# Optimization experiments

Hardware: AMD Instinct MI355X
Metric: run time of the kernel (lower is better)

## Reference

```python
import jax, jax.numpy as jnp
import numpy as np

B, F, R, P, C = 2048, 64, 32, 16, 128  # batch, nfeature(dsym), nrole, npattern, dcontext
TAU = 2.0  # posn_attender sharpness


def setup_inputs() -> dict:
    key = jax.random.key(0)
    ks = jax.random.split(key, 16)
    w = lambda k, shape, s=0.05: jax.random.normal(k, shape, jnp.float32) * s
    z = lambda shape: jnp.zeros(shape, jnp.float32)
    return {
        "form": jax.random.normal(ks[0], (B, F, R), jnp.float32),
        "context": jax.random.normal(ks[1], (B, C), jnp.float32),
        "mod_W": w(ks[2], (C, P * 6)), "mod_b": z((P * 6,)),
        "wch_W": w(ks[3], (C, P * F)), "wch_b": z((P * F,)),
        "wdl_W": w(ks[4], (C, P)), "wdl_b": z((P,)),
        "wep_W": w(ks[5], (C, P * 4)), "wep_b": z((P * 4,)),
        "vch_W": w(ks[6], (C, P * F)), "vch_b": z((P * F,)),
        "vep_W": w(ks[7], (C, P * F * 4)), "vep_b": z((P * F * 4,)),
        "wnc_W": w(ks[8], (C, F)), "wnc_b": z((F,)),
        "wnd_W": w(ks[9], (C, 1)), "wnd_b": z((1,)),
        "wne_W": w(ks[10], (C, 1)), "wne_b": z((1,)),
        "m_W": w(ks[11], (3, C, P * F)), "m_Wb": z((3, P * F)),
        "mb_W": w(ks[12], (3, C, P)), "mb_b": z((3, P)),
    }


def _forward(form, context, mod_W, mod_b, wch_W, wch_b, wdl_W, wdl_b,
             wep_W, wep_b, vch_W, vch_b, vep_W, vep_b,
             wnc_W, wnc_b, wnd_W, wnd_b, wne_W, wne_b,
             m_W, m_Wb, mb_W, mb_b):
    nb = form.shape[0]
    lin = lambda W, b: context @ W + b

    # context-conditioned rule weights
    mod = jax.nn.softmax(lin(mod_W, mod_b).reshape(nb, P, 6), axis=-1)
    w_chng = mod[..., 0:1] * lin(wch_W, wch_b).reshape(nb, P, F)
    w_deln = mod[..., 1:2] * lin(wdl_W, wdl_b).reshape(nb, P, 1)
    w_epen = mod[..., 2:] * lin(wep_W, wep_b).reshape(nb, P, 4)
    v_chng = lin(vch_W, vch_b).reshape(nb, P, F)
    v_epen = lin(vep_W, vep_b).reshape(nb, P, F, 4)
    w_nochng = jnp.exp(lin(wnc_W, wnc_b))   # (B, F)
    w_nodeln = jnp.exp(lin(wnd_W, wnd_b))   # (B, 1)
    w_noepen = jnp.exp(lin(wne_W, wne_b))   # (B, 1)

    # Matcher3: trigram (prev, cur, next) feature matching; log-prob summed then exp'd
    prev = jnp.pad(form[:, :, :-1], ((0, 0), (0, 0), (1, 0)))
    nxt = jnp.pad(form[:, :, 1:], ((0, 0), (0, 0), (0, 1)))
    forms3 = jnp.stack([prev, form, nxt], 0)                                   # (3,B,F,R)
    Wk = (jnp.einsum('bc,kcn->kbn', context, m_W) + m_Wb[:, None, :]).reshape(3, nb, P, F)
    bk = jnp.einsum('bc,kcp->kbp', context, mb_W) + mb_b[:, None, :]
    score = jnp.einsum('kbpf,kbfr->kbpr', Wk, forms3) + bk[..., None]
    match = jnp.exp(jnp.sum(jax.nn.log_sigmoid(score), axis=0))                # (B,P,R)

    positions = jnp.arange(R, dtype=form.dtype)

    def posn_attn(posn):  # (B,1) soft position -> (B,R) radial-basis attention
        return jax.nn.softmax(-TAU * (posn - positions[None, :]) ** 2, axis=-1)

    def bind(out, x, attn):  # soft write symbol x at attended role
        a = attn[:, None, :]
        return out * (1.0 - a) + x[:, :, None] * a

    def epen(out, posn, match_i, we_p, ve_p):
        we = match_i * we_p                                                    # (B,P)
        p = jax.nn.sigmoid(jnp.sum(we, 1, keepdims=True) - w_noepen)           # (B,1)
        v = jnp.sum(jax.nn.relu(we)[..., None] * ve_p, 1)                      # (B,F)
        out_ = bind(out, v, posn_attn(posn))
        out = p[..., None] * out_ + (1.0 - p[..., None]) * out
        return out, posn + p

    def step(carry, x):
        out, posn = carry
        sym_i, match_i = x  # (B,F), (B,P)
        # epenthesis before
        out, posn = epen(out, posn, match_i, w_epen[..., 0], v_epen[..., 0])
        # feature change + deletion
        wc = match_i[..., None] * w_chng                                       # (B,P,F)
        p_chng = jax.nn.sigmoid(jnp.sum(wc, 1) - w_nochng)                     # (B,F)
        vc = jnp.sum(jax.nn.relu(wc) * v_chng, 1)                              # (B,F)
        sym = sym_i + p_chng * (vc - sym_i)
        out_ = bind(out, sym, posn_attn(posn))
        wd = match_i[..., None] * w_deln                                       # (B,P,1)
        p_deln = jax.nn.sigmoid(jnp.sum(wd, 1) - w_nodeln)                     # (B,1)
        out = (1.0 - p_deln[..., None]) * out_ + p_deln[..., None] * out
        posn = posn + (1.0 - p_deln)
        # epenthesis after
        out, posn = epen(out, posn, match_i, w_epen[..., 2], v_epen[..., 2])
        return (out, posn), None

    carry0 = (jnp.zeros((nb, F, R), form.dtype), jnp.zeros((nb, 1), form.dtype))
    xs = (jnp.moveaxis(form, 2, 0), jnp.moveaxis(match, 2, 0))
    (out, _), _ = jax.lax.scan(step, carry0, xs)
    return out


def reference(form, context, mod_W, mod_b, wch_W, wch_b, wdl_W, wdl_b,
              wep_W, wep_b, vch_W, vch_b, vep_W, vep_b,
              wnc_W, wnc_b, wnd_W, wnd_b, wne_W, wne_b,
              m_W, m_Wb, mb_W, mb_b):
    return _forward(form, context, mod_W, mod_b, wch_W, wch_b, wdl_W, wdl_b,
                    wep_W, wep_b, vch_W, vch_b, vep_W, vep_b,
                    wnc_W, wnc_b, wnd_W, wnd_b, wne_W, wne_b,
                    m_W, m_Wb, mb_W, mb_b)
```

## Files before the change

kernel.cpp:

```cpp
#include <hip/hip_runtime.h>

#define B_ 2048
#define YS3 7440
#define NT  465

typedef unsigned short u16;
typedef unsigned int   u32;
typedef __attribute__((ext_vector_type(2))) float v2f;
typedef __attribute__((ext_vector_type(8))) short bf16x8;
typedef __attribute__((ext_vector_type(4))) float f32x4;

__device__ __forceinline__ float bfu(u16 u) {
    u32 i = ((u32)u) << 16; float f; __builtin_memcpy(&f, &i, 4); return f;
}
__device__ __forceinline__ u16 f2bf(float v) {
    u32 iv; __builtin_memcpy(&iv, &v, 4);
    u32 r = (iv + 0x7fffu + ((iv >> 16) & 1u)) >> 16;
    return (u16)r;
}
__device__ __forceinline__ float sigm(float x) { return 1.f / (1.f + __expf(-x)); }
__device__ __forceinline__ float lsg(float x) {
    return fminf(x, 0.f) - log1pf(__expf(-fabsf(x)));
}

template<bool F32> __device__ __forceinline__ float LD(const void* p, int e) {
    if (F32) return ((const float*)p)[e];
    return bfu(((const u16*)p)[e]);
}
template<bool F32> __device__ __forceinline__ float2 LD2(const void* p, int e) {
    if (F32) { const float* q = (const float*)p; return make_float2(q[e], q[e + 1]); }
    u32 w = ((const u32*)p)[e >> 1];
    u32 lo = w << 16, hi = w & 0xffff0000u; float a, b;
    __builtin_memcpy(&a, &lo, 4); __builtin_memcpy(&b, &hi, 4);
    return make_float2(a, b);
}
template<bool F32> __device__ __forceinline__ float4 LD4(const void* p, int e) {
    if (F32) return ((const float4*)p)[e >> 2];
    uint2 w = ((const uint2*)p)[e >> 2];
    u32 a0 = w.x << 16, a1 = w.x & 0xffff0000u, a2 = w.y << 16, a3 = w.y & 0xffff0000u;
    float f0, f1, f2, f3;
    __builtin_memcpy(&f0, &a0, 4); __builtin_memcpy(&f1, &a1, 4);
    __builtin_memcpy(&f2, &a2, 4); __builtin_memcpy(&f3, &a3, 4);
    return make_float4(f0, f1, f2, f3);
}
template<bool F32> __device__ __forceinline__ void ST(void* p, int e, float v) {
    if (F32) ((float*)p)[e] = v; else ((u16*)p)[e] = f2bf(v);
}

struct Args {
    const void *form, *ctx;
    const void *mod_W, *mod_b, *wch_W, *wch_b, *wdl_W, *wdl_b, *wep_W, *wep_b;
    const void *vch_W, *vch_b, *vep_W, *vep_b;
    const void *wnc_W, *wnc_b, *wnd_W, *wnd_b, *wne_W, *wne_b;
    const void *m_W, *m_Wb, *mb_W, *mb_b;
    void* outp;
};

__device__ __forceinline__ int probe_is_f32(const void* ctx, int t, int* flag_s) {
    if (t == 0) {
        int sane = 0;
        const u16* q = (const u16*)ctx;
        for (int i = 0; i < 64; ++i) {
            u16 u = q[2 * i];
            int ex = (u >> 7) & 0xFF;
            sane += (u == 0 || (ex >= 112 && ex <= 143)) ? 1 : 0;
        }
        *flag_s = (sane < 32) ? 1 : 0;
    }
    __syncthreads();
    return *flag_s;
}

__device__ __forceinline__ void split_bf16(float x, u16& hi, u16& lo) {
    hi = f2bf(x);
    lo = f2bf(x - bfu(hi));
}


template<bool F32>
__device__ void packw_body(int g, const Args& A, u16* Bpack, float* bcat) {
    int l  = g & 63;
    int kb = (g >> 6) & 3;
    int T  = g >> 8;
    int n  = T * 16 + (l & 15);
    int k0 = kb * 32 + (l >> 4) * 8;

    const void* p = A.wch_W; int off = 0, st = 0, zero = 0; float bb = 0.f;
    if (n < 1024)      { off = n; st = 1024; bb = LD<F32>(A.wch_b, n); }
    else if (n < 2048) { int j = n - 1024; p = A.vch_W; off = j; st = 1024; bb = LD<F32>(A.vch_b, j); }
    else if (n < 4096) { int i = n - 2048; int col = 4 * (i >> 1) + 2 * (i & 1);
                         p = A.vep_W; off = col; st = 4096; bb = LD<F32>(A.vep_b, col); }
    else if (n < 7168) { int i = n - 4096; int kk = i >> 10, j = i & 1023;
                         p = A.m_W; off = kk * 131072 + j; st = 1024; bb = LD<F32>(A.m_Wb, kk * 1024 + j); }
    else if (n < 7264) { int m = n - 7168; p = A.mod_W; off = m; st = 96; bb = LD<F32>(A.mod_b, m); }
    else if (n < 7312) { int i = n - 7264; int k = i >> 4, pp = i & 15;
                         p = A.mb_W; off = k * 2048 + pp; st = 16; bb = LD<F32>(A.mb_b, k * 16 + pp); }
    else if (n < 7344) { int i = n - 7312; int col = 4 * (i >> 1) + 2 * (i & 1);
                         p = A.wep_W; off = col; st = 64; bb = LD<F32>(A.wep_b, col); }
    else if (n < 7360) { int j = n - 7344; p = A.wdl_W; off = j; st = 16; bb = LD<F32>(A.wdl_b, j); }
    else if (n < 7424) { int j = n - 7360; p = A.wnc_W; off = j; st = 64; bb = LD<F32>(A.wnc_b, j); }
    else if (n == 7424){ p = A.wnd_W; off = 0; st = 1; bb = LD<F32>(A.wnd_b, 0); }
    else if (n == 7425){ p = A.wne_W; off = 0; st = 1; bb = LD<F32>(A.wne_b, 0); }
    else zero = 1;

    u16 hi[8], lo[8];
    #pragma unroll
    for (int j = 0; j < 8; ++j) {
        float w = LD<F32>(p, off + (k0 + j) * st);
        if (zero) w = 0.f;
        split_bf16(w, hi[j], lo[j]);
    }
    *(uint4*)(Bpack + ((size_t)T * 512 + kb * 64 + l) * 8)       = *(const uint4*)hi;
    *(uint4*)(Bpack + ((size_t)T * 512 + 256 + kb * 64 + l) * 8) = *(const uint4*)lo;
    if (kb == 0 && l < 16) bcat[n] = zero ? 0.f : bb;
}

__global__ __launch_bounds__(256) void packw_kernel(Args A, u16* Bpack, float* bcat) {
    __shared__ int dt_s;
    const int t = threadIdx.x;
    int isf32 = probe_is_f32(A.ctx, t, &dt_s);
    int g = blockIdx.x * 256 + t;
    if (isf32) packw_body<true>(g, A, Bpack, bcat);
    else       packw_body<false>(g, A, Bpack, bcat);
}

template<bool F32>
__device__ void gemm_mfma_body(float* As, int t, int blk, const void* __restrict__ ctx,
                               const u16* __restrict__ Bpack,
                               const float* __restrict__ bcat, float* __restrict__ Y) {
    const int l  = t & 63;
    const int w  = t >> 6;
    const int Mt = blk & 127;
    const int nb = blk >> 7;

    {
        int row = t >> 4, c0 = (t & 15) * 8;
        float4 x = LD4<F32>(ctx, (Mt * 16 + row) * 128 + c0);
        float4 y = LD4<F32>(ctx, (Mt * 16 + row) * 128 + c0 + 4);
        *(float4*)&As[row * 132 + c0]     = x;
        *(float4*)&As[row * 132 + c0 + 4] = y;
    }
    __syncthreads();

    bf16x8 ahi[4], alo[4];
    const int m = l & 15;
    #pragma unroll
    for (int kb = 0; kb < 4; ++kb) {
        int k0 = kb * 32 + (l >> 4) * 8;
        const float* ap = &As[m * 132 + k0];
        #pragma unroll
        for (int j = 0; j < 8; ++j) {
            u16 hi, lo; split_bf16(ap[j], hi, lo);
            ahi[kb][j] = (short)hi;
            alo[kb][j] = (short)lo;
        }
    }

    const int Tbase = nb * 16 + w * 4;
    const int row0  = Mt * 16 + (l >> 4) * 4;
    const int ncol  = l & 15;

    #pragma unroll
    for (int T = 0; T < 4; ++T) {
        int Tt = Tbase + T;
        if (Tt >= NT) break;
        const u16* Bb = Bpack + (size_t)Tt * 4096;
        bf16x8 bhi[4], blo[4];
        #pragma unroll
        for (int kb = 0; kb < 4; ++kb) {
            bhi[kb] = *(const bf16x8*)(Bb + ((kb) * 64 + l) * 8);
            blo[kb] = *(const bf16x8*)(Bb + ((4 + kb) * 64 + l) * 8);
        }
        f32x4 d = {0.f, 0.f, 0.f, 0.f};
        #pragma unroll
        for (int kb = 0; kb < 4; ++kb) {
            d = __builtin_amdgcn_mfma_f32_16x16x32_bf16(ahi[kb], bhi[kb], d, 0, 0, 0);
            d = __builtin_amdgcn_mfma_f32_16x16x32_bf16(ahi[kb], blo[kb], d, 0, 0, 0);
            d = __builtin_amdgcn_mfma_f32_16x16x32_bf16(alo[kb], bhi[kb], d, 0, 0, 0);
        }
        int n = Tt * 16 + ncol;
        float bv = bcat[n];
        #pragma unroll
        for (int i = 0; i < 4; ++i) {
            Y[(size_t)(row0 + i) * YS3 + n] = d[i] + bv;
        }
    }
}

__global__ __launch_bounds__(256) void gemm_mfma_kernel(Args A, const u16* Bpack,
                                                        const float* bcat, float* Y) {
    __shared__ float As[16 * 132];
    __shared__ int dt_s;
    const int t = threadIdx.x, blk = blockIdx.x;
    int isf32 = probe_is_f32(A.ctx, t, &dt_s);
    if (isf32) gemm_mfma_body<true>(As, t, blk, A.ctx, Bpack, bcat, Y);
    else       gemm_mfma_body<false>(As, t, blk, A.ctx, Bpack, bcat, Y);
}

struct __align__(16) ScanSmem {
    float U[6144];
    float V[3072];
    float match_s[512];
    float wnc_s[64];
    float wep0_s[16], wep2_s[16], wdl_s[16];
    float coef_s[96];
    float sc_s[2];
};

template<bool F32>
__device__ void scan_body(ScanSmem& S, int t, int b, const Args& A, const float* __restrict__ Y) {
    float* Wk_s   = S.U;
    float* bk_s   = S.U + 3072;
    float* modl   = S.U + 3120;
    float* form_s = S.U + 3312;
    float* xtab   = S.U;
    float* wch_s  = S.V;
    float* vch_s  = S.V + 1024;
    float* rlI    = S.V + 2048;
    float* gtab   = S.V;

    const float* Yr = Y + (size_t)b * YS3;
    const float4* Y4 = (const float4*)Yr;

    const int f_own = t & 63;
    const int fq    = t >> 6;

    const float2* vep2p = (const float2*)(Yr + 2048);
    v2f vepf[16];
    #pragma unroll
    for (int p = 0; p < 16; ++p) {
        float2 v = vep2p[p * 64 + f_own];
        vepf[p].x = v.x; vepf[p].y = v.y;
    }

    {
        int e0 = b * 2048 + t * 8;
        float4 x = LD4<F32>(A.form, e0);
        float4 y = LD4<F32>(A.form, e0 + 4);
        int f = t >> 2, r0 = (t & 3) * 8;
        float* dst = form_s + f * 33 + r0;
        dst[0] = x.x; dst[1] = x.y; dst[2] = x.z; dst[3] = x.w;
        dst[4] = y.x; dst[5] = y.y; dst[6] = y.z; dst[7] = y.w;
    }
    for (int i = t; i < 768; i += 256) ((float4*)Wk_s)[i] = Y4[1024 + i];
    if (t < 12) ((float4*)bk_s)[t] = Y4[1816 + t];
    if (t < 24) ((float4*)modl)[t] = Y4[1792 + t];
    ((float4*)wch_s)[t] = Y4[t];
    ((float4*)vch_s)[t] = Y4[256 + t];
    if (t < 16) {
        S.wep0_s[t] = Yr[7312 + 2 * t];
        S.wep2_s[t] = Yr[7312 + 2 * t + 1];
        S.wdl_s[t]  = Yr[7344 + t];
    } else if (t >= 32 && t < 96) {
        S.wnc_s[t - 32] = __expf(Yr[7360 + (t - 32)]);
    } else if (t >= 96 && t < 98) {
        S.sc_s[t - 96] = __expf(Yr[7424 + (t - 96)]);
    }
    __syncthreads();

    if (t < 16) {
        float v[6]; float mx = -1e30f;
        #pragma unroll
        for (int j = 0; j < 6; ++j) { v[j] = modl[t * 6 + j]; mx = fmaxf(mx, v[j]); }
        float s = 0.f;
        #pragma unroll
        for (int j = 0; j < 6; ++j) { v[j] = __expf(v[j] - mx); s += v[j]; }
        float inv = 1.f / s;
        #pragma unroll
        for (int j = 0; j < 6; ++j) modl[t * 6 + j] = v[j] * inv;
    }
    __syncthreads();

    if (t < 16) {
        S.wep0_s[t] *= modl[t * 6 + 2];
        S.wep2_s[t] *= modl[t * 6 + 4];
        S.wdl_s[t]  *= modl[t * 6 + 1];
    }
    for (int i = t; i < 1024; i += 256) wch_s[i] *= modl[(i >> 6) * 6];

    const int my_r = t & 31;
    #pragma unroll 1
    for (int it = 0; it < 2; ++it) {
        int idx = t + 256 * it;
        int p = idx >> 5, r = idx & 31;
        float s0 = bk_s[p], s1 = bk_s[16 + p], s2 = bk_s[32 + p];
        const float4* w0 = (const float4*)(Wk_s + p * 64);
        const float4* w1 = (const float4*)(Wk_s + (16 + p) * 64);
        const float4* w2 = (const float4*)(Wk_s + (32 + p) * 64);
        for (int f4 = 0; f4 < 16; ++f4) {
            float a0[4], a1[4], a2[4];
            *(float4*)a0 = w0[f4]; *(float4*)a1 = w1[f4]; *(float4*)a2 = w2[f4];
            #pragma unroll
            for (int j = 0; j < 4; ++j) {
                int f = f4 * 4 + j;
                float f0 = form_s[f * 33 + r];
                float fm = __shfl_up(f0, 1, 32);   if (r == 0)  fm = 0.f;
                float fp = __shfl_down(f0, 1, 32); if (r == 31) fp = 0.f;
                s0 += a0[j] * fm; s1 += a1[j] * f0; s2 += a2[j] * fp;
            }
        }
        S.match_s[p * 32 + r] = __expf(lsg(s0) + lsg(s1) + lsg(s2));
    }
    __syncthreads();

    if (t < 96) {
        int sub = t >> 5, r = t & 31;
        const float* w = (sub == 0) ? S.wep0_s : (sub == 1) ? S.wdl_s : S.wep2_s;
        float s = 0.f;
        for (int p = 0; p < 16; ++p) s += S.match_s[p * 32 + r] * w[p];
        float cf;
        if (sub == 1) cf = 1.f - sigm(s - S.sc_s[0]);
        else          cf = sigm(s - S.sc_s[1]);
        S.coef_s[sub * 32 + r] = cf;
    }
    for (int i = t; i < 512; i += 256) {
        int p = i >> 5, r = i & 31;
        float m = S.match_s[p * 32 + r];
        rlI[2 * i]     = fmaxf(m * S.wep0_s[p], 0.f);
        rlI[2 * i + 1] = fmaxf(m * S.wep2_s[p], 0.f);
    }
    float wchf[16], vchf[16];
    #pragma unroll
    for (int p = 0; p < 16; ++p) {
        wchf[p] = wch_s[p * 64 + f_own];
        vchf[p] = vch_s[p * 64 + f_own];
    }
    const float wncf = S.wnc_s[f_own];
    float si_r[8];
    #pragma unroll
    for (int j = 0; j < 8; ++j) si_r[j] = form_s[f_own * 33 + fq * 8 + j];
    __syncthreads();

    #pragma unroll 1
    for (int j = 0; j < 8; ++j) {
        int rs = fq * 8 + j;
        v2f v02; v02.x = 0.f; v02.y = 0.f;
        float sum = 0.f, vs1 = 0.f;
        const v2f* rlp = (const v2f*)(rlI + 2 * rs);
        #pragma unroll
        for (int p = 0; p < 16; ++p) {
            v2f rl = rlp[p * 32];
            v02 += rl * vepf[p];
            float m = S.match_s[p * 32 + rs];
            float wc = m * wchf[p];
            sum += wc;
            vs1 += fmaxf(wc, 0.f) * vchf[p];
        }
        float pch = sigm(sum - wncf);
        float si  = si_r[j];
        xtab[0 * 2048 + rs * 64 + f_own] = v02.x;
        xtab[1 * 2048 + rs * 64 + f_own] = si + pch * (vs1 - si);
        xtab[2 * 2048 + rs * 64 + f_own] = v02.y;
    }
    __syncthreads();

    float* ck_s  = S.match_s;
    float* pos_s = S.match_s + 128;
    if (t < 96) ck_s[t] = S.coef_s[(t % 3) * 32 + (t / 3)];
    __syncthreads();
    if (t < 64) {
        float a = ck_s[t];
        float a0 = a;
        #pragma unroll
        for (int d = 1; d < 64; d <<= 1) { float v = __shfl_up(a, d, 64); if (t >= d) a += v; }
        pos_s[t] = a - a0;
        float carry = __shfl(a, 63, 64);
        float b2 = (t < 32) ? ck_s[64 + t] : 0.f;
        float c2 = b2;
        #pragma unroll
        for (int d = 1; d < 32; d <<= 1) { float v = __shfl_up(c2, d, 32); if ((t & 31) >= d) c2 += v; }
        if (t < 32) pos_s[64 + t] = carry + c2 - b2;
    }
    __syncthreads();

    #pragma unroll 1
    for (int i = 0; i < 12; ++i) {
        int idx = t + 256 * i;
        int k = idx >> 5, r = idx & 31;
        float posn = pos_s[k];
        float pc = fminf(posn, 31.f);
        float ci = floorf(pc + 0.5f);
        float dmin = posn - ci;
        float dd = posn - (float)r;
        float eo = __expf(-2.f * (dd * dd - dmin * dmin));
        float Z = eo;
        Z += __shfl_xor(Z, 1, 32);
        Z += __shfl_xor(Z, 2, 32);
        Z += __shfl_xor(Z, 4, 32);
        Z += __shfl_xor(Z, 8, 32);
        Z += __shfl_xor(Z, 16, 32);
        gtab[idx] = ck_s[k] * eo / Z;
    }
    __syncthreads();

    const int fgrp = t >> 5;
    v2f o01, o23, o45, o67;
    o01 = 0.f; o23 = 0.f; o45 = 0.f; o67 = 0.f;
    #pragma unroll 1
    for (int rs = 0; rs < 32; ++rs) {
        #pragma unroll
        for (int sub = 0; sub < 3; ++sub) {
            float g = gtab[(rs * 3 + sub) * 32 + my_r];
            v2f gv; gv.x = g; gv.y = g;
            const float4* xb = (const float4*)(xtab + sub * 2048 + rs * 64 + fgrp * 8);
            float4 xa = xb[0], xc = xb[1];
            v2f x01, x23, x45, x67;
            x01.x = xa.x; x01.y = xa.y; x23.x = xa.z; x23.y = xa.w;
            x45.x = xc.x; x45.y = xc.y; x67.x = xc.z; x67.y = xc.w;
            o01 += gv * (x01 - o01);
            o23 += gv * (x23 - o23);
            o45 += gv * (x45 - o45);
            o67 += gv * (x67 - o67);
        }
    }

    float oreg[8] = {o01.x, o01.y, o23.x, o23.y, o45.x, o45.y, o67.x, o67.y};
    #pragma unroll
    for (int i = 0; i < 8; ++i) {
        ST<F32>(A.outp, b * 2048 + (fgrp * 8 + i) * 32 + my_r, oreg[i]);
    }
}

__global__ __launch_bounds__(256) void scan_kernel(Args A, const float* Y) {
    __shared__ ScanSmem S;
    __shared__ int dt_s;
    const int t = threadIdx.x, b = blockIdx.x;
    int isf32 = probe_is_f32(A.ctx, t, &dt_s);
    if (isf32) scan_body<true>(S, t, b, A, Y);
    else       scan_body<false>(S, t, b, A, Y);
}

struct Smem {
    float U[6144];
    float form_s[64 * 33];
    float match_s[512];
    float wch_s[1024];
    float vch_s[1024];
    float vep0_s[1024];
    float vep2_s[1024];
    float wep0_s[16], wep2_s[16], wdl_s[16];
    float wnc_s[64];
    float sc_s[2];
    float ssum_s[96];
};

template<bool F32>
__device__ void mono_body(Smem& S, int t, int b, const Args& A) {
    float* c_s  = S.U;
    float* modl = S.U + 128;
    float* Wk_s = S.U + 224;
    float* bk_s = S.U + 3344;
    float* xtab = S.U;

    if (t < 128) c_s[t] = LD<F32>(A.ctx, b * 128 + t);
    {
        int e0 = b * 2048 + t * 8;
        float4 x = LD4<F32>(A.form, e0);
        float4 y = LD4<F32>(A.form, e0 + 4);
        int f = t >> 2, r0 = (t & 3) * 8;
        float* dst = S.form_s + f * 33 + r0;
        dst[0] = x.x; dst[1] = x.y; dst[2] = x.z; dst[3] = x.w;
        dst[4] = y.x; dst[5] = y.y; dst[6] = y.z; dst[7] = y.w;
    }
    __syncthreads();
    if (t < 96) {
        float a = LD<F32>(A.mod_b, t);
        for (int cc = 0; cc < 128; ++cc) a += c_s[cc] * LD<F32>(A.mod_W, cc * 96 + t);
        modl[t] = a;
    }
    __syncthreads();
    if (t < 16) {
        float v[6]; float mx = -1e30f;
        #pragma unroll
        for (int j = 0; j < 6; ++j) { v[j] = modl[t * 6 + j]; mx = fmaxf(mx, v[j]); }
        float s = 0.f;
        #pragma unroll
        for (int j = 0; j < 6; ++j) { v[j] = __expf(v[j] - mx); s += v[j]; }
        float inv = 1.f / s;
        #pragma unroll
        for (int j = 0; j < 6; ++j) modl[t * 6 + j] = v[j] * inv;
    }
    __syncthreads();
    for (int j = t; j < 512; j += 256) {
        int n0 = j * 2;
        float2 bb = LD2<F32>(A.wch_b, n0);
        float a0 = bb.x, a1 = bb.y;
        for (int cc = 0; cc < 128; ++cc) {
            float2 w = LD2<F32>(A.wch_W, cc * 1024 + n0); float cv = c_s[cc];
            a0 += cv * w.x; a1 += cv * w.y;
        }
        int p = n0 >> 6; float sc = modl[p * 6 + 0];
        S.wch_s[n0] = sc * a0; S.wch_s[n0 + 1] = sc * a1;
    }
    for (int j = t; j < 512; j += 256) {
        int n0 = j * 2;
        float2 bb = LD2<F32>(A.vch_b, n0);
        float a0 = bb.x, a1 = bb.y;
        for (int cc = 0; cc < 128; ++cc) {
            float2 w = LD2<F32>(A.vch_W, cc * 1024 + n0); float cv = c_s[cc];
            a0 += cv * w.x; a1 += cv * w.y;
        }
        S.vch_s[n0] = a0; S.vch_s[n0 + 1] = a1;
    }
    for (int u = t; u < 1024; u += 256) {
        int n0 = u * 4;
        float4 bb = LD4<F32>(A.vep_b, n0);
        float a0 = bb.x, a2 = bb.z;
        for (int cc = 0; cc < 128; ++cc) {
            float4 w = LD4<F32>(A.vep_W, cc * 4096 + n0); float cv = c_s[cc];
            a0 += cv * w.x; a2 += cv * w.z;
        }
        S.vep0_s[u] = a0; S.vep2_s[u] = a2;
    }
    for (int j = t; j < 1536; j += 256) {
        int k  = j >> 9;
        int jj = j & 511;
        int n0 = jj * 2;
        float2 bb = LD2<F32>(A.m_Wb, k * 1024 + n0);
        float a0 = bb.x, a1 = bb.y;
        for (int cc = 0; cc < 128; ++cc) {
            float2 w = LD2<F32>(A.m_W, (k * 128 + cc) * 1024 + n0); float cv = c_s[cc];
            a0 += cv * w.x; a1 += cv * w.y;
        }
        int p = n0 >> 6, f = n0 & 63;
        Wk_s[(k * 16 + p) * 65 + f]     = a0;
        Wk_s[(k * 16 + p) * 65 + f + 1] = a1;
    }
    if (t < 16) {
        int n0 = t * 4;
        float4 bb = LD4<F32>(A.wep_b, n0);
        float a0 = bb.x, a2 = bb.z;
        for (int cc = 0; cc < 128; ++cc) {
            float4 w = LD4<F32>(A.wep_W, cc * 64 + n0); float cv = c_s[cc];
            a0 += cv * w.x; a2 += cv * w.z;
        }
        S.wep0_s[t] = modl[t * 6 + 2] * a0;
        S.wep2_s[t] = modl[t * 6 + 4] * a2;
    } else if (t < 32) {
        int p = t - 16;
        float a = LD<F32>(A.wdl_b, p);
        for (int cc = 0; cc < 128; ++cc) a += c_s[cc] * LD<F32>(A.wdl_W, cc * 16 + p);
        S.wdl_s[p] = modl[p * 6 + 1] * a;
    } else if (t < 96) {
        int f = t - 32;
        float a = LD<F32>(A.wnc_b, f);
        for (int cc = 0; cc < 128; ++cc) a += c_s[cc] * LD<F32>(A.wnc_W, cc * 64 + f);
        S.wnc_s[f] = __expf(a);
    } else if (t < 98) {
        const void* W  = (t == 96) ? A.wnd_W : A.wne_W;
        const void* bb = (t == 96) ? A.wnd_b : A.wne_b;
        float a = LD<F32>(bb, 0);
        for (int cc = 0; cc < 128; ++cc) a += c_s[cc] * LD<F32>(W, cc);
        S.sc_s[t - 96] = __expf(a);
    } else if (t < 146) {
        int i = t - 98;
        int k = i >> 4, p = i & 15;
        float a = LD<F32>(A.mb_b, k * 16 + p);
        for (int cc = 0; cc < 128; ++cc) a += c_s[cc] * LD<F32>(A.mb_W, (k * 128 + cc) * 16 + p);
        bk_s[i] = a;
    }
    __syncthreads();
    for (int idx = t; idx < 512; idx += 256) {
        int p = idx >> 5, r = idx & 31;
        float s0 = bk_s[p], s1 = bk_s[16 + p], s2 = bk_s[32 + p];
        const float* w0 = Wk_s + p * 65;
        const float* w1 = Wk_s + (16 + p) * 65;
        const float* w2 = Wk_s + (32 + p) * 65;
        for (int f = 0; f < 64; ++f) {
            const float* fr = S.form_s + f * 33 + r;
            float fm1 = (r > 0)  ? fr[-1] : 0.f;
            float f0  = fr[0];
            float fp1 = (r < 31) ? fr[1]  : 0.f;
            s0 += w0[f] * fm1; s1 += w1[f] * f0; s2 += w2[f] * fp1;
        }
        S.match_s[p * 32 + r] = __expf(lsg(s0) + lsg(s1) + lsg(s2));
    }
    __syncthreads();
    if (t < 96) {
        int which = t >> 5, r = t & 31;
        const float* w = (which == 0) ? S.wep0_s : (which == 1) ? S.wep2_s : S.wdl_s;
        float s = 0.f;
        for (int p = 0; p < 16; ++p) s += S.match_s[p * 32 + r] * w[p];
        S.ssum_s[which * 32 + r] = s;
    }
    #pragma unroll 1
    for (int q = 0; q < 24; ++q) {
        int idx = t + 256 * q;
        int sub = idx >> 11;
        int rs  = (idx >> 6) & 31;
        int f   = idx & 63;
        float x;
        if (sub == 1) {
            float sum = 0.f, vs = 0.f;
            for (int p = 0; p < 16; ++p) {
                float wc = S.match_s[p * 32 + rs] * S.wch_s[p * 64 + f];
                sum += wc;
                vs  += fmaxf(wc, 0.f) * S.vch_s[p * 64 + f];
            }
            float pch = sigm(sum - S.wnc_s[f]);
            float si  = S.form_s[f * 33 + rs];
            x = si + pch * (vs - si);
        } else {
            const float* wep = (sub == 0) ? S.wep0_s : S.wep2_s;
            const float* vep = (sub == 0) ? S.vep0_s : S.vep2_s;
            float vs = 0.f;
            for (int p = 0; p < 16; ++p) {
                float w = S.match_s[p * 32 + rs] * wep[p];
                vs += fmaxf(w, 0.f) * vep[p * 64 + f];
            }
            x = vs;
        }
        xtab[idx] = x;
    }
    __syncthreads();
    const int my_r = t & 31;
    const int fgrp = t >> 5;
    float oreg[8];
    #pragma unroll
    for (int i = 0; i < 8; ++i) oreg[i] = 0.f;
    float posn = 0.f;
    const float wnd1v = S.sc_s[0];
    const float wne1v = S.sc_s[1];
    for (int rs = 0; rs < 32; ++rs) {
        #pragma unroll
        for (int sub = 0; sub < 3; ++sub) {
            float coef;
            if (sub == 1) coef = 1.f - sigm(S.ssum_s[64 + rs] - wnd1v);
            else          coef = sigm(S.ssum_s[(sub & 2) * 16 + rs] - wne1v);
            float pc = fminf(posn, 31.f);
            int ci = (int)(pc + 0.5f);
            int lo = ci - 4; if (lo < 0)  lo = 0;
            int hi = ci + 4; if (hi > 31) hi = 31;
            float dmin = posn - (float)ci;
            float mx = -2.f * dmin * dmin;
            float Z = 0.f, eo = 0.f;
            for (int r = lo; r <= hi; ++r) {
                float d = posn - (float)r;
                float e = __expf(-2.f * d * d - mx);
                Z += e;
                if (r == my_r) eo = e;
            }
            float g = coef * eo / Z;
            const float* xb = xtab + (sub * 2048 + rs * 64 + fgrp * 8);
            #pragma unroll
            for (int i = 0; i < 8; ++i) oreg[i] += g * (xb[i] - oreg[i]);
            posn += coef;
        }
    }
    #pragma unroll
    for (int i = 0; i < 8; ++i) {
        ST<F32>(A.outp, b * 2048 + (fgrp * 8 + i) * 32 + my_r, oreg[i]);
    }
}

__global__ __launch_bounds__(256) void phon_mono(Args A) {
    __shared__ Smem S;
    __shared__ int dt_s;
    const int t = threadIdx.x, b = blockIdx.x;
    int isf32 = probe_is_f32(A.ctx, t, &dt_s);
    if (isf32) mono_body<true>(S, t, b, A);
    else       mono_body<false>(S, t, b, A);
}

extern "C" void kernel_launch(void* const* d_in, const int* in_sizes, int n_in,
                              void* d_out, int out_size, void* d_ws, size_t ws_size,
                              hipStream_t stream) {
    Args A;
    A.form  = d_in[0];  A.ctx   = d_in[1];
    A.mod_W = d_in[2];  A.mod_b = d_in[3];
    A.wch_W = d_in[4];  A.wch_b = d_in[5];
    A.wdl_W = d_in[6];  A.wdl_b = d_in[7];
    A.wep_W = d_in[8];  A.wep_b = d_in[9];
    A.vch_W = d_in[10]; A.vch_b = d_in[11];
    A.vep_W = d_in[12]; A.vep_b = d_in[13];
    A.wnc_W = d_in[14]; A.wnc_b = d_in[15];
    A.wnd_W = d_in[16]; A.wnd_b = d_in[17];
    A.wne_W = d_in[18]; A.wne_b = d_in[19];
    A.m_W   = d_in[20]; A.m_Wb  = d_in[21];
    A.mb_W  = d_in[22]; A.mb_b  = d_in[23];
    A.outp  = d_out;

    const size_t yElems  = (size_t)B_ * YS3;
    const size_t bpElems = (size_t)NT * 4096;
    const size_t need = yElems * 4 + bpElems * 2 + (size_t)YS3 * 4;
    if (ws_size >= need) {
        float* Y     = (float*)d_ws;
        u16*   Bpack = (u16*)(Y + yElems);
        float* bcat  = (float*)(Bpack + bpElems);
        packw_kernel<<<NT, 256, 0, stream>>>(A, Bpack, bcat);
        gemm_mfma_kernel<<<30 * 128, 256, 0, stream>>>(A, Bpack, bcat, Y);
        scan_kernel<<<B_, 256, 0, stream>>>(A, Y);
    } else {
        phon_mono<<<B_, 256, 0, stream>>>(A);
    }
}
```

Before: 243.8 us.

## Compute trigram matcher with split-bf16 MFMA and vectorize xtab accumulation

Replaces the scalar FMA/shuffle trigram matching loop with 16x16x32 bf16 MFMAs, using hi/lo bf16 splitting (three products) to keep near-fp32 accuracy. Matcher weights are now read straight from global memory instead of being staged in shared memory, and form_s is padded with zero columns so the shifted prev/next operands need no shuffles. The per-rs loop that builds xtab is restructured to accumulate all 8 rows at once with float4 LDS reads, and the vep register loads are moved later to ease register pressure. The cost is extra conversion arithmetic and the small error of the three-term bf16 split.

```diff
diff --git a/kernel.cpp b/kernel.cpp
--- a/kernel.cpp
+++ b/kernel.cpp
@@ -209,10 +209,9 @@
 
 template<bool F32>
 __device__ void scan_body(ScanSmem& S, int t, int b, const Args& A, const float* __restrict__ Y) {
-    float* Wk_s   = S.U;
-    float* bk_s   = S.U + 3072;
-    float* modl   = S.U + 3120;
-    float* form_s = S.U + 3312;
+    float* bk_s   = S.U;
+    float* modl   = S.U + 48;
+    float* form_s = S.U + 144;
     float* xtab   = S.U;
     float* wch_s  = S.V;
     float* vch_s  = S.V + 1024;
@@ -224,37 +223,33 @@
 
     const int f_own = t & 63;
     const int fq    = t >> 6;
-
-    const float2* vep2p = (const float2*)(Yr + 2048);
-    v2f vepf[16];
-    #pragma unroll
-    for (int p = 0; p < 16; ++p) {
-        float2 v = vep2p[p * 64 + f_own];
-        vepf[p].x = v.x; vepf[p].y = v.y;
-    }
-
+    const int l     = t & 63;
+    const int wv    = t >> 6;
+    const int my_r  = t & 31;
+
+    if (t < 64) { form_s[t * 34] = 0.f; form_s[t * 34 + 33] = 0.f; }
     {
         int e0 = b * 2048 + t * 8;
         float4 x = LD4<F32>(A.form, e0);
         float4 y = LD4<F32>(A.form, e0 + 4);
         int f = t >> 2, r0 = (t & 3) * 8;
-        float* dst = form_s + f * 33 + r0;
+        float* dst = form_s + f * 34 + 1 + r0;
         dst[0] = x.x; dst[1] = x.y; dst[2] = x.z; dst[3] = x.w;
         dst[4] = y.x; dst[5] = y.y; dst[6] = y.z; dst[7] = y.w;
     }
-    for (int i = t; i < 768; i += 256) ((float4*)Wk_s)[i] = Y4[1024 + i];
     if (t < 12) ((float4*)bk_s)[t] = Y4[1816 + t];
-    if (t < 24) ((float4*)modl)[t] = Y4[1792 + t];
+    else if (t >= 32 && t < 56) ((float4*)modl)[t - 32] = Y4[1792 + (t - 32)];
     ((float4*)wch_s)[t] = Y4[t];
     ((float4*)vch_s)[t] = Y4[256 + t];
-    if (t < 16) {
-        S.wep0_s[t] = Yr[7312 + 2 * t];
-        S.wep2_s[t] = Yr[7312 + 2 * t + 1];
-        S.wdl_s[t]  = Yr[7344 + t];
-    } else if (t >= 32 && t < 96) {
-        S.wnc_s[t - 32] = __expf(Yr[7360 + (t - 32)]);
-    } else if (t >= 96 && t < 98) {
-        S.sc_s[t - 96] = __expf(Yr[7424 + (t - 96)]);
+    if (t >= 64 && t < 80) {
+        int p = t - 64;
+        S.wep0_s[p] = Yr[7312 + 2 * p];
+        S.wep2_s[p] = Yr[7312 + 2 * p + 1];
+        S.wdl_s[p]  = Yr[7344 + p];
+    } else if (t >= 96 && t < 160) {
+        S.wnc_s[t - 96] = __expf(Yr[7360 + (t - 96)]);
+    } else if (t >= 160 && t < 162) {
+        S.sc_s[t - 160] = __expf(Yr[7424 + (t - 160)]);
     }
     __syncthreads();
 
@@ -278,28 +273,46 @@
     }
     for (int i = t; i < 1024; i += 256) wch_s[i] *= modl[(i >> 6) * 6];
 
-    const int my_r = t & 31;
-    #pragma unroll 1
-    for (int it = 0; it < 2; ++it) {
-        int idx = t + 256 * it;
-        int p = idx >> 5, r = idx & 31;
-        float s0 = bk_s[p], s1 = bk_s[16 + p], s2 = bk_s[32 + p];
-        const float4* w0 = (const float4*)(Wk_s + p * 64);
-        const float4* w1 = (const float4*)(Wk_s + (16 + p) * 64);
-        const float4* w2 = (const float4*)(Wk_s + (32 + p) * 64);
-        for (int f4 = 0; f4 < 16; ++f4) {
-            float a0[4], a1[4], a2[4];
-            *(float4*)a0 = w0[f4]; *(float4*)a1 = w1[f4]; *(float4*)a2 = w2[f4];
+    if (wv < 2) {
+        const int q  = l >> 4;
+        const int rb = wv * 16 + (l & 15);
+        f32x4 msum = {0.f, 0.f, 0.f, 0.f};
+        #pragma unroll
+        for (int kmat = 0; kmat < 3; ++kmat) {
+            f32x4 d = {0.f, 0.f, 0.f, 0.f};
             #pragma unroll
-            for (int j = 0; j < 4; ++j) {
-                int f = f4 * 4 + j;
-                float f0 = form_s[f * 33 + r];
-                float fm = __shfl_up(f0, 1, 32);   if (r == 0)  fm = 0.f;
-                float fp = __shfl_down(f0, 1, 32); if (r == 31) fp = 0.f;
-                s0 += a0[j] * fm; s1 += a1[j] * f0; s2 += a2[j] * fp;
+            for (int kb = 0; kb < 2; ++kb) {
+                const float* ap = Yr + 4096 + kmat * 1024 + (l & 15) * 64 + kb * 32 + q * 8;
+                float4 a0 = *(const float4*)ap;
+                float4 a1 = *(const float4*)(ap + 4);
+                float av[8] = {a0.x, a0.y, a0.z, a0.w, a1.x, a1.y, a1.z, a1.w};
+                bf16x8 Ahi, Alo, Bhi, Blo;
+                #pragma unroll
+                for (int j = 0; j < 8; ++j) {
+                    u16 hi, lo; split_bf16(av[j], hi, lo);
+                    Ahi[j] = (short)hi; Alo[j] = (short)lo;
+                }
+                int coladdr = rb + kmat;
+                #pragma unroll
+                for (int j = 0; j < 8; ++j) {
+                    int f = kb * 32 + q * 8 + j;
+                    float v = form_s[f * 34 + coladdr];
+                    u16 hi, lo; split_bf16(v, hi, lo);
+                    Bhi[j] = (short)hi; Blo[j] = (short)lo;
+                }
+                d = __builtin_amdgcn_mfma_f32_16x16x32_bf16(Ahi, Bhi, d, 0, 0, 0);
+                d = __builtin_amdgcn_mfma_f32_16x16x32_bf16(Ahi, Blo, d, 0, 0, 0);
+                d = __builtin_amdgcn_mfma_f32_16x16x32_bf16(Alo, Bhi, d, 0, 0, 0);
             }
-        }
-        S.match_s[p * 32 + r] = __expf(lsg(s0) + lsg(s1) + lsg(s2));
+            #pragma unroll
+            for (int i = 0; i < 4; ++i) {
+                msum[i] += lsg(d[i] + bk_s[kmat * 16 + q * 4 + i]);
+            }
+        }
+        #pragma unroll
+        for (int i = 0; i < 4; ++i) {
+            S.match_s[(q * 4 + i) * 32 + rb] = __expf(msum[i]);
+        }
     }
     __syncthreads();
 
@@ -319,6 +332,13 @@
         rlI[2 * i]     = fmaxf(m * S.wep0_s[p], 0.f);
         rlI[2 * i + 1] = fmaxf(m * S.wep2_s[p], 0.f);
     }
+    const float2* vep2p = (const float2*)(Yr + 2048);
+    v2f vepf[16];
+    #pragma unroll
+    for (int p = 0; p < 16; ++p) {
+        float2 v = vep2p[p * 64 + f_own];
+        vepf[p].x = v.x; vepf[p].y = v.y;
+    }
     float wchf[16], vchf[16];
     #pragma unroll
     for (int p = 0; p < 16; ++p) {
@@ -328,29 +348,41 @@
     const float wncf = S.wnc_s[f_own];
     float si_r[8];
     #pragma unroll
-    for (int j = 0; j < 8; ++j) si_r[j] = form_s[f_own * 33 + fq * 8 + j];
-    __syncthreads();
-
-    #pragma unroll 1
-    for (int j = 0; j < 8; ++j) {
-        int rs = fq * 8 + j;
-        v2f v02; v02.x = 0.f; v02.y = 0.f;
-        float sum = 0.f, vs1 = 0.f;
-        const v2f* rlp = (const v2f*)(rlI + 2 * rs);
+    for (int j = 0; j < 8; ++j) si_r[j] = form_s[f_own * 34 + 1 + fq * 8 + j];
+    __syncthreads();
+
+    {
+        v2f v02[8]; float sum[8], vs1[8];
+        #pragma unroll
+        for (int j = 0; j < 8; ++j) { v02[j].x = 0.f; v02[j].y = 0.f; sum[j] = 0.f; vs1[j] = 0.f; }
+        const float4* m4  = (const float4*)S.match_s;
+        const float4* rl4 = (const float4*)rlI;
         #pragma unroll
         for (int p = 0; p < 16; ++p) {
-            v2f rl = rlp[p * 32];
-            v02 += rl * vepf[p];
-            float m = S.match_s[p * 32 + rs];
-            float wc = m * wchf[p];
-            sum += wc;
-            vs1 += fmaxf(wc, 0.f) * vchf[p];
-        }
-        float pch = sigm(sum - wncf);
-        float si  = si_r[j];
-        xtab[0 * 2048 + rs * 64 + f_own] = v02.x;
-        xtab[1 * 2048 + rs * 64 + f_own] = si + pch * (vs1 - si);
-        xtab[2 * 2048 + rs * 64 + f_own] = v02.y;
+            float4 ma = m4[p * 8 + fq * 2], mb = m4[p * 8 + fq * 2 + 1];
+            float mm[8] = {ma.x, ma.y, ma.z, ma.w, mb.x, mb.y, mb.z, mb.w};
+            float4 ra = rl4[p * 16 + fq * 4],     rb2 = rl4[p * 16 + fq * 4 + 1];
+            float4 rc = rl4[p * 16 + fq * 4 + 2], rd  = rl4[p * 16 + fq * 4 + 3];
+            float rl[16] = {ra.x, ra.y, ra.z, ra.w, rb2.x, rb2.y, rb2.z, rb2.w,
+                            rc.x, rc.y, rc.z, rc.w, rd.x, rd.y, rd.z, rd.w};
+            #pragma unroll
+            for (int j = 0; j < 8; ++j) {
+                v02[j].x += rl[2 * j]     * vepf[p].x;
+                v02[j].y += rl[2 * j + 1] * vepf[p].y;
+                float wc = mm[j] * wchf[p];
+                sum[j] += wc;
+                vs1[j] += fmaxf(wc, 0.f) * vchf[p];
+            }
+        }
+        #pragma unroll
+        for (int j = 0; j < 8; ++j) {
+            int rs = fq * 8 + j;
+            float pch = sigm(sum[j] - wncf);
+            float si  = si_r[j];
+            xtab[rs * 64 + f_own]        = v02[j].x;
+            xtab[2048 + rs * 64 + f_own] = si + pch * (vs1[j] - si);
+            xtab[4096 + rs * 64 + f_own] = v02[j].y;
+        }
     }
     __syncthreads();
 
```

Result: faster. 236.0 us (-3.2%).
